# Optimization experiments

Measured on AMD Instinct MI355X. Metric: run time of the kernel, lower is better.

## Reference

```python
import jax, jax.numpy as jnp
import numpy as np

N_BLADES = 8      # 2**len(sig_g), sig_g=[1,1,1]
N_EP_STEPS = 3
STEP_SIZE = 0.01
B, IN_DIM, OUT_DIM = 1024, 4096, 2048
HID = OUT_DIM * N_BLADES


def setup_inputs() -> dict:
    key = jax.random.key(0)
    k0, k1, k2, k3, k4, k5 = jax.random.split(key, 6)
    x = jax.random.normal(k0, (B, IN_DIM), jnp.float32)
    # input_proj: Linear(in_dim, out_dim*n_blades)
    W_in = jax.random.normal(k1, (IN_DIM, HID), jnp.float32) / np.sqrt(IN_DIM)
    b_in = jax.random.normal(k2, (HID,), jnp.float32) * 0.01
    # energy interaction matrix W: (n_blades, n_blades), init * 0.1
    W_e = jax.random.normal(k3, (N_BLADES, N_BLADES), jnp.float32) * 0.1
    # output_proj: Linear(out_dim*n_blades, out_dim)
    W_out = jax.random.normal(k4, (HID, OUT_DIM), jnp.float32) / np.sqrt(HID)
    b_out = jax.random.normal(k5, (OUT_DIM,), jnp.float32) * 0.01
    return {"x": x, "W_in": W_in, "b_in": b_in, "W_e": W_e,
            "W_out": W_out, "b_out": b_out}


def reference(x, W_in, b_in, W_e, W_out, b_out):
    # h: (B, out_dim, n_blades)
    h = (x @ W_in + b_in).reshape(x.shape[0], OUT_DIM, N_BLADES)
    # EP relaxation: analytic dE/dh = h + 0.1 * h @ (W + W^T)
    # (torch computed this via autograd on a detached copy each step,
    #  so the gradient term carries no graph -> stop_gradient)
    W_sym = W_e + W_e.T
    for _ in range(N_EP_STEPS):
        grad = jax.lax.stop_gradient(h + 0.1 * (h @ W_sym))
        h = h - STEP_SIZE * grad
    h_flat = h.reshape(x.shape[0], HID)
    return h_flat @ W_out + b_out
```

## Files before the change

kernel.cpp:

```cpp
#include <hip/hip_runtime.h>
#include <stdint.h>

#define AS1 __attribute__((address_space(1)))
#define AS3 __attribute__((address_space(3)))

typedef float v4f __attribute__((ext_vector_type(4)));
typedef __bf16 v8bf __attribute__((ext_vector_type(8)));
typedef __bf16 bf16x4 __attribute__((ext_vector_type(4)));

static_assert(sizeof(v8bf) == 16, "v8bf must be 16B");
static_assert(sizeof(bf16x4) == 8, "bf16x4 must be 8B");

__device__ __forceinline__ unsigned short f2bf(float f) {
  unsigned int x = __float_as_uint(f);
  x += 0x7fffu + ((x >> 16) & 1u);
  return (unsigned short)(x >> 16);
}

__device__ __forceinline__ void async16(void* lds, const void* g) {
  __builtin_amdgcn_global_load_lds((const AS1 unsigned int*)g,
                                   (AS3 unsigned int*)lds, 16, 0, 0);
}


__global__ void prep_m3_kernel(const float* __restrict__ We, float* __restrict__ m3) {
  __shared__ float Ms[64], M2[64];
  int t = threadIdx.x;
  int i = t >> 3, j = t & 7;
  float wsym = We[i * 8 + j] + We[j * 8 + i];
  Ms[t] = (i == j ? 0.99f : 0.0f) - 0.001f * wsym;
  __syncthreads();
  float s = 0.f;
#pragma unroll
  for (int p = 0; p < 8; ++p) s += Ms[i * 8 + p] * Ms[p * 8 + j];
  M2[t] = s;
  __syncthreads();
  s = 0.f;
#pragma unroll
  for (int p = 0; p < 8; ++p) s += M2[i * 8 + p] * Ms[p * 8 + j];
  m3[t] = s;
}

__global__ void cvt_bf16_kernel(const float* __restrict__ in, unsigned short* __restrict__ out) {
  int i = (blockIdx.x * 256 + threadIdx.x) * 8;
  float4 a = *(const float4*)(in + i);
  float4 b = *(const float4*)(in + i + 4);
  alignas(16) unsigned short r[8] = {f2bf(a.x), f2bf(a.y), f2bf(a.z), f2bf(a.w),
                                     f2bf(b.x), f2bf(b.y), f2bf(b.z), f2bf(b.w)};
  *(uint4*)(out + i) = *(const uint4*)r;
}

__global__ void fold_h_kernel(unsigned short* __restrict__ h, const float* __restrict__ m3) {
  __shared__ float m3s[64];
  int t = threadIdx.x;
  if (t < 64) m3s[t] = m3[t];
  __syncthreads();
  size_t g = ((size_t)blockIdx.x * 256 + t) * 8;
  uint4 raw = *(const uint4*)(h + g);
  const unsigned short* rp = (const unsigned short*)&raw;
  float v[8];
#pragma unroll
  for (int p = 0; p < 8; ++p) v[p] = __uint_as_float((unsigned int)rp[p] << 16);
  alignas(16) unsigned short o[8];
#pragma unroll
  for (int j = 0; j < 8; ++j) {
    float s = 0.f;
#pragma unroll
    for (int p = 0; p < 8; ++p) s += v[p] * m3s[p * 8 + j];
    o[j] = f2bf(s);
  }
  *(uint4*)(h + g) = *(const uint4*)o;
}

template <bool OUT_BF16, bool SPLITK>
__global__ __launch_bounds__(512, 1) void gemm256f_kernel(
    const unsigned short* __restrict__ A, const float* __restrict__ Bsrc,
    const float* __restrict__ bias, void* __restrict__ Cout,
    int M, int N, int K, int ldkA, int ldnB) {
  __shared__ char ldsc[131072];

  const int flat = blockIdx.x + gridDim.x * (blockIdx.y + gridDim.y * blockIdx.z);
  const int xcd = flat & 7, idx = flat >> 3;
  int bn, bm, bz;
  if (SPLITK) { bz = xcd; bn = idx & 7; bm = idx >> 3; }
  else        { bz = 0;   bn = xcd * 8 + (idx & 7); bm = idx >> 3; }
  const int m0 = bm * 256, n0 = bn * 256;
  const int kb = SPLITK ? bz * K : 0;

  const int t = threadIdx.x;
  const int lane = t & 63, w = t >> 6;
  const int wr = w >> 2, wn = w & 3;
  const int r16 = lane & 15, kc = lane >> 4;
  const int xorv = (r16 & 7) << 4;
  const int acol0 = (kc << 4) ^ xorv;
  const int acol1 = ((4 | kc) << 4) ^ xorv;
  const int abase = wr * 16384 + r16 * 128;
  const int bbase = 32768 + wn * 8192 + r16 * 128;

  const int srow = w * 8 + (lane >> 3);
  const int scol = ((lane & 7) ^ (lane >> 3)) * 8;
  const int sdst = w * 1024 + lane * 16;
  const unsigned short* gAp = A + (size_t)(m0 + srow) * ldkA + kb + scol;

  const int n0s = 4 * lane;
  const int rotc = (lane >> 1) & 3;
  const float* gB = Bsrc + (size_t)(kb + w * 4) * ldnB + n0 + n0s;

  v4f acc[8][4];
#pragma unroll
  for (int mi = 0; mi < 8; ++mi)
#pragma unroll
    for (int nj = 0; nj < 4; ++nj) acc[mi][nj] = (v4f){0.f, 0.f, 0.f, 0.f};

  float4 L[2][4];

#define STAGE_A(OB)                                                        \
  _Pragma("unroll") for (int i = 0; i < 4; ++i)                            \
      async16(ldsc + (OB) + i * 8192 + sdst, gAp + (size_t)(i * 64) * ldkA);
#define LOAD_BGLB()                                                        \
  _Pragma("unroll") for (int ii = 0; ii < 2; ++ii)                         \
      _Pragma("unroll") for (int j = 0; j < 4; ++j)                        \
          L[ii][j] = *(const float4*)(gB + (size_t)(ii * 32 + j) * ldnB);
#define CVT_WRITE_B(OB)                                                          \
  _Pragma("unroll") for (int ii = 0; ii < 2; ++ii) {                             \
    const int k4 = w * 4 + ii * 32;                                              \
    bf16x4 R0 = (bf16x4){(__bf16)L[ii][0].x, (__bf16)L[ii][1].x,                 \
                         (__bf16)L[ii][2].x, (__bf16)L[ii][3].x};                \
    bf16x4 R1 = (bf16x4){(__bf16)L[ii][0].y, (__bf16)L[ii][1].y,                 \
                         (__bf16)L[ii][2].y, (__bf16)L[ii][3].y};                \
    bf16x4 R2 = (bf16x4){(__bf16)L[ii][0].z, (__bf16)L[ii][1].z,                 \
                         (__bf16)L[ii][2].z, (__bf16)L[ii][3].z};                \
    bf16x4 R3 = (bf16x4){(__bf16)L[ii][0].w, (__bf16)L[ii][1].w,                 \
                         (__bf16)L[ii][2].w, (__bf16)L[ii][3].w};                \
    _Pragma("unroll") for (int d = 0; d < 4; ++d) {                              \
      int o = (d + rotc) & 3;                                                    \
      int row = n0s + o;                                                         \
      bf16x4 vv = (o & 2) ? ((o & 1) ? R3 : R2) : ((o & 1) ? R1 : R0);           \
      *(bf16x4*)(ldsc + (OB) + 32768 + row * 128 +                               \
                 ((((k4 >> 3) ^ (row & 7)) << 4) | ((k4 & 7) << 1))) = vv;       \
    }                                                                            \
  }
#define LOAD_A(BB, MH)                                                     \
  _Pragma("unroll") for (int m = 0; m < 4; ++m) {                          \
    a[m * 2 + 0] = *(const v8bf*)(ldsc + (BB) + abase + (MH) * 8192 + m * 2048 + acol0); \
    a[m * 2 + 1] = *(const v8bf*)(ldsc + (BB) + abase + (MH) * 8192 + m * 2048 + acol1); \
  }
#define LOAD_B(BB, NH, BR)                                                 \
  _Pragma("unroll") for (int n = 0; n < 2; ++n) {                          \
    BR[n * 2 + 0] = *(const v8bf*)(ldsc + (BB) + bbase + (NH) * 4096 + n * 2048 + acol0); \
    BR[n * 2 + 1] = *(const v8bf*)(ldsc + (BB) + bbase + (NH) * 4096 + n * 2048 + acol1); \
  }
#define MFMA_QUAD(MH, NH, BR)                                              \
  _Pragma("unroll") for (int m = 0; m < 4; ++m) {                          \
    _Pragma("unroll") for (int n = 0; n < 2; ++n) {                        \
      acc[(MH) * 4 + m][(NH) * 2 + n] = __builtin_amdgcn_mfma_f32_16x16x32_bf16( \
          a[m * 2 + 0], BR[n * 2 + 0], acc[(MH) * 4 + m][(NH) * 2 + n], 0, 0, 0); \
      acc[(MH) * 4 + m][(NH) * 2 + n] = __builtin_amdgcn_mfma_f32_16x16x32_bf16( \
          a[m * 2 + 1], BR[n * 2 + 1], acc[(MH) * 4 + m][(NH) * 2 + n], 0, 0, 0); \
    }                                                                      \
  }

  const int NT = K >> 6;

  STAGE_A(0);
  LOAD_BGLB();
  gAp += 64;
  CVT_WRITE_B(0);
  if (NT > 1) gB += (size_t)64 * ldnB;
  LOAD_BGLB();
  if (NT > 2) gB += (size_t)64 * ldnB;
  asm volatile("s_waitcnt vmcnt(8) lgkmcnt(0)" ::: "memory");
  __builtin_amdgcn_s_barrier();

  int buf = 0;
  for (int tt = 0; tt < NT; ++tt) {
    const int bb = buf << 16;
    const int ob = (buf ^ 1) << 16;
    const bool pf = (tt + 1 < NT);

    if (pf) {
      CVT_WRITE_B(ob);
      STAGE_A(ob);
      gAp += 64;
    }
    LOAD_BGLB();
    if (tt + 3 < NT) gB += (size_t)64 * ldnB;
    __builtin_amdgcn_sched_barrier(0);

    {
      v8bf a[8], b0r[4], b1r[4];
      LOAD_A(bb, 0);
      LOAD_B(bb, 0, b0r);
      MFMA_QUAD(0, 0, b0r);
      LOAD_B(bb, 1, b1r);
      MFMA_QUAD(0, 1, b1r);
      LOAD_A(bb, 1);
      MFMA_QUAD(1, 1, b1r);
      LOAD_B(bb, 0, b0r);
      MFMA_QUAD(1, 0, b0r);
    }
    __builtin_amdgcn_sched_barrier(0);

    asm volatile("s_waitcnt vmcnt(8) lgkmcnt(0)" ::: "memory");
    __builtin_amdgcn_s_barrier();
    buf ^= 1;
  }

  float* Cp = (float*)Cout + (SPLITK ? (size_t)bz * M * N : 0);
#pragma unroll
  for (int mi = 0; mi < 8; ++mi) {
    int grow = m0 + wr * 128 + mi * 16 + kc * 4;
#pragma unroll
    for (int nj = 0; nj < 4; ++nj) {
      int gcol = n0 + wn * 64 + nj * 16 + r16;
      float bv = SPLITK ? 0.f : bias[gcol];
#pragma unroll
      for (int j = 0; j < 4; ++j) {
        float v = acc[mi][nj][j] + bv;
        size_t idxo = (size_t)(grow + j) * N + gcol;
        if (OUT_BF16)
          ((unsigned short*)Cout)[idxo] = f2bf(v);
        else
          Cp[idxo] = v;
      }
    }
  }
#undef STAGE_A
#undef LOAD_BGLB
#undef CVT_WRITE_B
#undef LOAD_A
#undef LOAD_B
#undef MFMA_QUAD
}

__global__ void reduce_splitk_kernel(const float* __restrict__ part,
                                     const float* __restrict__ bias,
                                     float* __restrict__ out, int MN, int N, int S) {
  int i = (blockIdx.x * 256 + threadIdx.x) * 4;
  float4 s = *(const float4*)(part + i);
  for (int k = 1; k < S; ++k) {
    float4 v = *(const float4*)(part + (size_t)k * MN + i);
    s.x += v.x; s.y += v.y; s.z += v.z; s.w += v.w;
  }
  int n = i & (N - 1);
  const float4 bv = *(const float4*)(bias + n);
  s.x += bv.x; s.y += bv.y; s.z += bv.z; s.w += bv.w;
  *(float4*)(out + i) = s;
}


extern "C" void kernel_launch(void* const* d_in, const int* in_sizes, int n_in,
                              void* d_out, int out_size, void* d_ws, size_t ws_size,
                              hipStream_t stream) {
  const float* x     = (const float*)d_in[0];
  const float* W_in  = (const float*)d_in[1];
  const float* b_in  = (const float*)d_in[2];
  const float* W_e   = (const float*)d_in[3];
  const float* W_out = (const float*)d_in[4];
  const float* b_out = (const float*)d_in[5];
  float* out = (float*)d_out;

  char* ws = (char*)d_ws;
  const size_t OFF_M3 = 0;
  const size_t OFF_X  = 1ull << 20;
  const size_t OFF_H  = 10ull << 20;
  const size_t OFF_P  = 48ull << 20;
  float* m3          = (float*)(ws + OFF_M3);
  unsigned short* xb = (unsigned short*)(ws + OFF_X);
  unsigned short* h  = (unsigned short*)(ws + OFF_H);
  float* part        = (float*)(ws + OFF_P);

  prep_m3_kernel<<<1, 64, 0, stream>>>(W_e, m3);
  cvt_bf16_kernel<<<2048, 256, 0, stream>>>(x, xb);

  gemm256f_kernel<true, false><<<dim3(64, 4), 512, 0, stream>>>(
      xb, W_in, b_in, h, 1024, 16384, 4096, 4096, 16384);

  fold_h_kernel<<<8192, 256, 0, stream>>>(h, m3);

  gemm256f_kernel<false, true><<<dim3(8, 4, 8), 512, 0, stream>>>(
      h, W_out, nullptr, part, 1024, 2048, 2048, 16384, 2048);

  reduce_splitk_kernel<<<2048, 256, 0, stream>>>(part, b_out, out, 1024 * 2048, 2048, 8);
}
```

Baseline: 258.9 us.

## Split GEMM main loop into four barrier-synced phases interleaving loads with MFMA

Restructures the double-buffered GEMM inner loop into four phases. Each phase issues LDS reads and part of the next tile's global staging or convert-write, then runs one MFMA quadrant under raised wave priority, bracketed by workgroup barriers. The aim is to spread memory traffic across the MFMA work so waves overlap loads and math in a ping-pong style. It adds eight extra barriers per iteration, which may cost more than the overlap gains.

```diff
diff --git a/kernel.cpp b/kernel.cpp
--- a/kernel.cpp
+++ b/kernel.cpp
@@ -159,6 +159,14 @@
           a[m * 2 + 1], BR[n * 2 + 1], acc[(MH) * 4 + m][(NH) * 2 + n], 0, 0, 0); \
     }                                                                      \
   }
+#define PHASE_SYNC()                                          \
+  __builtin_amdgcn_s_barrier();                               \
+  asm volatile("s_waitcnt lgkmcnt(0)" ::: "memory");          \
+  __builtin_amdgcn_sched_barrier(0);                          \
+  __builtin_amdgcn_s_setprio(1);
+#define PHASE_END()                                           \
+  __builtin_amdgcn_s_setprio(0);                              \
+  __builtin_amdgcn_s_barrier();
 
   const int NT = K >> 6;
 
@@ -177,31 +185,35 @@
     const int bb = buf << 16;
     const int ob = (buf ^ 1) << 16;
     const bool pf = (tt + 1 < NT);
-
-    if (pf) {
-      CVT_WRITE_B(ob);
-      STAGE_A(ob);
-      gAp += 64;
-    }
+    v8bf a[8], b0r[4], b1r[4];
+
+    LOAD_A(bb, 0);
+    LOAD_B(bb, 0, b0r);
+    if (pf) { STAGE_A(ob); gAp += 64; }
+    PHASE_SYNC();
+    MFMA_QUAD(0, 0, b0r);
+    PHASE_END();
+
+    LOAD_B(bb, 1, b1r);
+    if (pf) { CVT_WRITE_B(ob); }
+    PHASE_SYNC();
+    MFMA_QUAD(0, 1, b1r);
+    PHASE_END();
+
+    LOAD_A(bb, 1);
     LOAD_BGLB();
     if (tt + 3 < NT) gB += (size_t)64 * ldnB;
+    PHASE_SYNC();
+    MFMA_QUAD(1, 1, b1r);
+    PHASE_END();
+
+    LOAD_B(bb, 0, b0r);
+    PHASE_SYNC();
+    MFMA_QUAD(1, 0, b0r);
+    PHASE_END();
+
+    asm volatile("s_waitcnt vmcnt(8)" ::: "memory");
     __builtin_amdgcn_sched_barrier(0);
-
-    {
-      v8bf a[8], b0r[4], b1r[4];
-      LOAD_A(bb, 0);
-      LOAD_B(bb, 0, b0r);
-      MFMA_QUAD(0, 0, b0r);
-      LOAD_B(bb, 1, b1r);
-      MFMA_QUAD(0, 1, b1r);
-      LOAD_A(bb, 1);
-      MFMA_QUAD(1, 1, b1r);
-      LOAD_B(bb, 0, b0r);
-      MFMA_QUAD(1, 0, b0r);
-    }
-    __builtin_amdgcn_sched_barrier(0);
-
-    asm volatile("s_waitcnt vmcnt(8) lgkmcnt(0)" ::: "memory");
     __builtin_amdgcn_s_barrier();
     buf ^= 1;
   }
@@ -231,6 +243,8 @@
 #undef LOAD_A
 #undef LOAD_B
 #undef MFMA_QUAD
+#undef PHASE_SYNC
+#undef PHASE_END
 }
 
 __global__ void reduce_splitk_kernel(const float* __restrict__ part,
```

After: 292.5 us. 13.0% more time.

## Store split-K partials in bf16 and move B conversion after MFMA block

Applied to the files above, without the earlier changes.

The split-K GEMM now writes its partial sums as bf16 rather than fp32, and the reduce kernel reads and sums bf16 partials. This halves the partial-buffer write and read traffic but adds rounding error to each partial. The main loop is also reordered. The B tile is converted and written, and the next B global load is issued, after the MFMA block rather than before it, so the global loads overlap the math. The redundant reload of B fragments is removed by keeping both B register sets live, which raises register pressure.

```diff
diff --git a/kernel.cpp b/kernel.cpp
--- a/kernel.cpp
+++ b/kernel.cpp
@@ -15,6 +15,10 @@
   unsigned int x = __float_as_uint(f);
   x += 0x7fffu + ((x >> 16) & 1u);
   return (unsigned short)(x >> 16);
+}
+
+__device__ __forceinline__ float bf2f(unsigned short u) {
+  return __uint_as_float((unsigned int)u << 16);
 }
 
 __device__ __forceinline__ void async16(void* lds, const void* g) {
@@ -60,7 +64,7 @@
   const unsigned short* rp = (const unsigned short*)&raw;
   float v[8];
 #pragma unroll
-  for (int p = 0; p < 8; ++p) v[p] = __uint_as_float((unsigned int)rp[p] << 16);
+  for (int p = 0; p < 8; ++p) v[p] = bf2f(rp[p]);
   alignas(16) unsigned short o[8];
 #pragma unroll
   for (int j = 0; j < 8; ++j) {
@@ -169,7 +173,7 @@
   if (NT > 1) gB += (size_t)64 * ldnB;
   LOAD_BGLB();
   if (NT > 2) gB += (size_t)64 * ldnB;
-  asm volatile("s_waitcnt vmcnt(8) lgkmcnt(0)" ::: "memory");
+  asm volatile("s_waitcnt lgkmcnt(0)" ::: "memory");
   __builtin_amdgcn_s_barrier();
 
   int buf = 0;
@@ -178,35 +182,34 @@
     const int ob = (buf ^ 1) << 16;
     const bool pf = (tt + 1 < NT);
 
-    if (pf) {
-      CVT_WRITE_B(ob);
-      STAGE_A(ob);
-      gAp += 64;
-    }
-    LOAD_BGLB();
-    if (tt + 3 < NT) gB += (size_t)64 * ldnB;
+    if (pf) { STAGE_A(ob); gAp += 64; }
     __builtin_amdgcn_sched_barrier(0);
 
     {
       v8bf a[8], b0r[4], b1r[4];
       LOAD_A(bb, 0);
       LOAD_B(bb, 0, b0r);
+      LOAD_B(bb, 1, b1r);
       MFMA_QUAD(0, 0, b0r);
-      LOAD_B(bb, 1, b1r);
       MFMA_QUAD(0, 1, b1r);
       LOAD_A(bb, 1);
       MFMA_QUAD(1, 1, b1r);
-      LOAD_B(bb, 0, b0r);
       MFMA_QUAD(1, 0, b0r);
     }
     __builtin_amdgcn_sched_barrier(0);
 
+    if (pf) { CVT_WRITE_B(ob); }
+    LOAD_BGLB();
+    if (tt + 3 < NT) gB += (size_t)64 * ldnB;
+    __builtin_amdgcn_sched_barrier(0);
+
     asm volatile("s_waitcnt vmcnt(8) lgkmcnt(0)" ::: "memory");
     __builtin_amdgcn_s_barrier();
     buf ^= 1;
   }
 
-  float* Cp = (float*)Cout + (SPLITK ? (size_t)bz * M * N : 0);
+  unsigned short* Pp =
+      (unsigned short*)Cout + (SPLITK ? (size_t)bz * M * N : 0);
 #pragma unroll
   for (int mi = 0; mi < 8; ++mi) {
     int grow = m0 + wr * 128 + mi * 16 + kc * 4;
@@ -220,8 +223,10 @@
         size_t idxo = (size_t)(grow + j) * N + gcol;
         if (OUT_BF16)
           ((unsigned short*)Cout)[idxo] = f2bf(v);
+        else if (SPLITK)
+          Pp[idxo] = f2bf(v);
         else
-          Cp[idxo] = v;
+          ((float*)Cout)[idxo] = v;
       }
     }
   }
@@ -233,14 +238,14 @@
 #undef MFMA_QUAD
 }
 
-__global__ void reduce_splitk_kernel(const float* __restrict__ part,
+__global__ void reduce_splitk_kernel(const unsigned short* __restrict__ part,
                                      const float* __restrict__ bias,
                                      float* __restrict__ out, int MN, int N, int S) {
   int i = (blockIdx.x * 256 + threadIdx.x) * 4;
-  float4 s = *(const float4*)(part + i);
-  for (int k = 1; k < S; ++k) {
-    float4 v = *(const float4*)(part + (size_t)k * MN + i);
-    s.x += v.x; s.y += v.y; s.z += v.z; s.w += v.w;
+  float4 s = {0.f, 0.f, 0.f, 0.f};
+  for (int k = 0; k < S; ++k) {
+    ushort4 v = *(const ushort4*)(part + (size_t)k * MN + i);
+    s.x += bf2f(v.x); s.y += bf2f(v.y); s.z += bf2f(v.z); s.w += bf2f(v.w);
   }
   int n = i & (N - 1);
   const float4 bv = *(const float4*)(bias + n);
@@ -268,7 +273,7 @@
   float* m3          = (float*)(ws + OFF_M3);
   unsigned short* xb = (unsigned short*)(ws + OFF_X);
   unsigned short* h  = (unsigned short*)(ws + OFF_H);
-  float* part        = (float*)(ws + OFF_P);
+  unsigned short* part = (unsigned short*)(ws + OFF_P);
 
   prep_m3_kernel<<<1, 64, 0, stream>>>(W_e, m3);
   cvt_bf16_kernel<<<2048, 256, 0, stream>>>(x, xb);
```

Result: faster. 252.4 us (-2.5%).
